# Optimization experiments

Hardware: AMD Instinct MI355X
Metric: run time of the kernel (lower is better)

Reference implementation:

```python
import jax, jax.numpy as jnp
import numpy as np

DOWN = 2
KCONV = 3

def _blur_kernel():
    # _setup_kernel([1,3,3,1]): outer product, normalize; is_ref flips it.
    k = np.array([1.0, 3.0, 3.0, 1.0], dtype=np.float32)
    K = np.outer(k, k)
    K /= K.sum()
    K = K[::-1, ::-1].copy()  # torch.flip(dims=(0,1)) (symmetric here, kept for fidelity)
    return jnp.asarray(K)  # [4,4]

def setup_inputs() -> dict:
    key = jax.random.key(0)
    k1, k2, k3 = jax.random.split(key, 3)
    x = jax.random.normal(k1, (16, 256, 128, 128), dtype=jnp.float32)
    weight = jax.random.normal(k2, (512, 256, KCONV, KCONV), dtype=jnp.float32)  # OIHW
    bias = jax.random.normal(k3, (512,), dtype=jnp.float32)
    return {"x": x, "weight": weight, "bias": bias, "blur_k": _blur_kernel()}

def reference(x, weight, bias, blur_k):
    N, C, H, W = x.shape
    Wb = blur_k.shape[-1]
    # pad sizes: p = Wb - down + (Wconv - 1)
    p = Wb - DOWN + (KCONV - 1)
    pad0, pad1 = (p + 1) // 2, p // 2
    # upfirdn_2d (up=down=1): pad + depthwise FIR correlation with the (pre-flipped) kernel
    kd = jnp.broadcast_to(blur_k[None, None], (C, 1, Wb, Wb))  # depthwise OIHW
    xb = jax.lax.conv_general_dilated(
        x, kd, window_strides=(1, 1),
        padding=[(pad0, pad1), (pad0, pad1)],
        feature_group_count=C,
        dimension_numbers=("NCHW", "OIHW", "NCHW"))  # [N,C,129,129]
    # EqualizedLRConv2d: runtime weight scaling 1/sqrt(fan_in), stride=2, no padding
    fan_in = weight.shape[1] * weight.shape[2] * weight.shape[3]
    scale = 1.0 / np.sqrt(fan_in)
    y = jax.lax.conv_general_dilated(
        xb, weight * jnp.float32(scale), window_strides=(DOWN, DOWN),
        padding="VALID",
        dimension_numbers=("NCHW", "OIHW", "NCHW"))  # [N,512,64,64]
    return y + bias[None, :, None, None]
```

## Files before the change

### kernel.cpp

```cpp
#include <hip/hip_runtime.h>
#include <hip/hip_bf16.h>
#include <stdint.h>
#include <stddef.h>

#define NB   16
#define CIN  256
#define HIN  128
#define WIN  128
#define COUT 512
#define HO   64
#define WO   64
#define HBL  129

typedef __attribute__((ext_vector_type(8))) __bf16 bf16x8;
typedef __attribute__((ext_vector_type(4))) float  f32x4;

__device__ __forceinline__ void gld_lds16(const void* g, void* l) {
  __builtin_amdgcn_global_load_lds(
      (const __attribute__((address_space(1))) void*)g,
      (__attribute__((address_space(3))) void*)l, 16, 0, 0);
}

__device__ __forceinline__ unsigned pack_bf16(float lo, float hi) {
  __hip_bfloat16 l = __float2bfloat16(lo), h = __float2bfloat16(hi);
  unsigned short ul = *(unsigned short*)&l, uh = *(unsigned short*)&h;
  return (unsigned)ul | ((unsigned)uh << 16);
}

__global__ __launch_bounds__(512) void blur_kernel(
    const float* __restrict__ x,
    const float* __restrict__ bk,
    __hip_bfloat16* __restrict__ xb)
{
  __shared__ __hip_bfloat16 lout[CIN * 130];

  const int bid0 = blockIdx.x;
  const int bid  = (bid0 & 7) * 258 + (bid0 >> 3);
  const int n    = bid / HBL;
  const int io   = bid % HBL;
  const int t    = threadIdx.x;
  const int wave = t >> 6;
  const int lane = t & 63;
  const int half = lane >> 5;
  const int g    = lane & 31;

  const float K11 = bk[5];
  float a[4], b[4];
  #pragma unroll
  for (int u = 0; u < 4; ++u) a[u] = bk[u * 4 + 1] / K11;
  #pragma unroll
  for (int v = 0; v < 4; ++v) b[v] = bk[4 + v];

  int rr[4];
  #pragma unroll
  for (int u = 0; u < 4; ++u) {
    int r = io - 2 + u;
    if (r < 0 || r >= HIN) { a[u] = 0.f; r = 0; }
    rr[u] = r;
  }

  #pragma unroll 2
  for (int cb = wave * 2; cb < CIN; cb += 16) {
    const int c = cb + half;
    const float4* xr = (const float4*)(x + ((size_t)(n * CIN + c) * HIN) * WIN);
    float4 vm = {0.f, 0.f, 0.f, 0.f};
    #pragma unroll
    for (int u = 0; u < 4; ++u) {
      const float4 rv = xr[rr[u] * 32 + g];
      vm.x += a[u] * rv.x; vm.y += a[u] * rv.y;
      vm.z += a[u] * rv.z; vm.w += a[u] * rv.w;
    }
    float vmm2 = __shfl_up(vm.z, 1);
    float vmm1 = __shfl_up(vm.w, 1);
    float vmp4 = __shfl_down(vm.x, 1);
    if (g == 0)  { vmm2 = 0.f; vmm1 = 0.f; }
    if (g == 31) { vmp4 = 0.f; }
    const float o0 = b[0]*vmm2 + b[1]*vmm1 + b[2]*vm.x + b[3]*vm.y;
    const float o1 = b[0]*vmm1 + b[1]*vm.x + b[2]*vm.y + b[3]*vm.z;
    const float o2 = b[0]*vm.x + b[1]*vm.y + b[2]*vm.z + b[3]*vm.w;
    const float o3 = b[0]*vm.y + b[1]*vm.z + b[2]*vm.w + b[3]*vmp4;
    unsigned* dst = (unsigned*)&lout[c * 130 + 4 * g];
    dst[0] = pack_bf16(o0, o1);
    dst[1] = pack_bf16(o2, o3);
    if (g == 31)
      lout[c * 130 + 128] = __float2bfloat16(b[0]*vm.z + b[1]*vm.w);
  }

  __syncthreads();

  const size_t obase = ((size_t)(n * HBL + io)) * HBL * CIN;
  for (int e = t; e < 65 * 64; e += 512) {
    const int jp = e >> 6;
    const int l  = e & 63;
    const unsigned r0 = *(const unsigned*)&lout[(4*l + 0) * 130 + 2*jp];
    const unsigned r1 = *(const unsigned*)&lout[(4*l + 1) * 130 + 2*jp];
    const unsigned r2 = *(const unsigned*)&lout[(4*l + 2) * 130 + 2*jp];
    const unsigned r3 = *(const unsigned*)&lout[(4*l + 3) * 130 + 2*jp];
    uint2 s0, s1;
    s0.x = (r0 & 0xffffu) | (r1 << 16);
    s0.y = (r2 & 0xffffu) | (r3 << 16);
    s1.x = (r0 >> 16) | (r1 & 0xffff0000u);
    s1.y = (r2 >> 16) | (r3 & 0xffff0000u);
    *(uint2*)&xb[obase + (size_t)(2*jp) * CIN + 4*l] = s0;
    if (jp < 64)
      *(uint2*)&xb[obase + (size_t)(2*jp + 1) * CIN + 4*l] = s1;
  }
}

__global__ __launch_bounds__(256) void wprep_kernel(
    const float* __restrict__ w,
    __hip_bfloat16* __restrict__ wt)
{
  const int idx = blockIdx.x * 256 + threadIdx.x;
  if (idx >= 9 * COUT * CIN) return;
  const int c   = idx & (CIN - 1);
  const int o   = (idx >> 8) & (COUT - 1);
  const int tap = idx >> 17;
  wt[idx] = __float2bfloat16(w[(o * CIN + c) * 9 + tap]);
}

__global__ void gemm_kernel(
    const __hip_bfloat16* __restrict__ xb,
    const __hip_bfloat16* __restrict__ wt,
    const float* __restrict__ bias,
    float* __restrict__ y)
{
  __shared__ __hip_bfloat16 sW[128 * 64];
  __shared__ __hip_bfloat16 sX[128 * 64];

  const int t    = threadIdx.x;
  const int wave = t >> 6;
  const int lane = t & 63;
  const int bid0 = blockIdx.x;
  const int bid  = (bid0 & 7) * 256 + (bid0 >> 3);
  const int nb   = bid & 3;
  const int mb   = bid >> 2;
  const int o0   = nb * 128;
  const int p0   = mb * 128;
  const int imgn = p0 >> 12;
  const int h0   = (p0 >> 6) & 63;

  const int lane_r = lane >> 3;
  const int lane_g = lane & 7;

  f32x4 acc[4][4];
  #pragma unroll
  for (int ai = 0; ai < 4; ++ai)
    #pragma unroll
    for (int bi = 0; bi < 4; ++bi)
      acc[ai][bi] = (f32x4){0.f, 0.f, 0.f, 0.f};

  long xconst[4], wconst[4];
  #pragma unroll
  for (int s = 0; s < 4; ++s) {
    const int r  = (wave * 4 + s) * 8 + lane_r;
    const int g  = lane_g ^ (r & 7);
    const int hh = h0 + (r >> 6);
    const int ww = r & 63;
    xconst[s] = ((long)(imgn * HBL + 2 * hh) * HBL + 2 * ww) * CIN + g * 8;
    wconst[s] = (long)(o0 + r) * CIN + g * 8;
  }

  const int q   = lane >> 4;
  const int m16 = lane & 15;
  const int ro_base = (wave >> 1) * 64;
  const int rp_base = (wave & 1) * 64;

  for (int tap = 0; tap < 9; ++tap) {
    const long xoff_tap = (long)((tap / 3) * HBL + (tap % 3)) * CIN;
    const long woff_tap = (long)tap * (COUT * CIN);
    for (int cb = 0; cb < CIN; cb += 64) {
      #pragma unroll
      for (int s = 0; s < 4; ++s) {
        const int issue = wave * 4 + s;
        gld_lds16(wt + woff_tap + wconst[s] + cb, (char*)sW + issue * 1024);
        gld_lds16(xb + xoff_tap + xconst[s] + cb, (char*)sX + issue * 1024);
      }
      asm volatile("s_waitcnt vmcnt(0)" ::: "memory");
      __syncthreads();

      #pragma unroll
      for (int kk = 0; kk < 2; ++kk) {
        bf16x8 af[4], bfr[4];
        #pragma unroll
        for (int i4 = 0; i4 < 4; ++i4) {
          const int ro = ro_base + i4 * 16 + m16;
          const int ga = (kk * 4 + q) ^ (ro & 7);
          af[i4] = *(const bf16x8*)((const char*)sW + ro * 128 + ga * 16);
          const int rp = rp_base + i4 * 16 + m16;
          const int gb = (kk * 4 + q) ^ (rp & 7);
          bfr[i4] = *(const bf16x8*)((const char*)sX + rp * 128 + gb * 16);
        }
        #pragma unroll
        for (int ai = 0; ai < 4; ++ai)
          #pragma unroll
          for (int bi = 0; bi < 4; ++bi)
            acc[ai][bi] = __builtin_amdgcn_mfma_f32_16x16x32_bf16(
                af[ai], bfr[bi], acc[ai][bi], 0, 0, 0);
      }
      __syncthreads();
    }
  }

  const float scale = 1.0f / 48.0f;
  #pragma unroll
  for (int ai = 0; ai < 4; ++ai) {
    const int o = o0 + (wave >> 1) * 64 + ai * 16 + q * 4;
    #pragma unroll
    for (int bi = 0; bi < 4; ++bi) {
      const int p  = p0 + (wave & 1) * 64 + bi * 16 + m16;
      const int n  = p >> 12;
      const int hh = (p >> 6) & 63;
      const int ww = p & 63;
      const size_t obase = ((size_t)(n * COUT + o) * HO + hh) * WO + ww;
      #pragma unroll
      for (int rg = 0; rg < 4; ++rg) {
        const float v = acc[ai][bi][rg] * scale + bias[o + rg];
        y[obase + (size_t)rg * (HO * WO)] = v;
      }
    }
  }
}

extern "C" void kernel_launch(void* const* d_in, const int* in_sizes, int n_in,
                              void* d_out, int out_size, void* d_ws, size_t ws_size,
                              hipStream_t stream) {
  const float* x  = (const float*)d_in[0];
  const float* w  = (const float*)d_in[1];
  const float* bs = (const float*)d_in[2];
  const float* bk = (const float*)d_in[3];
  float* y = (float*)d_out;

  __hip_bfloat16* xb = (__hip_bfloat16*)d_ws;
  __hip_bfloat16* wt = (__hip_bfloat16*)((char*)d_ws +
                       (size_t)NB * HBL * HBL * CIN * sizeof(__hip_bfloat16));

  hipLaunchKernelGGL(blur_kernel, dim3(NB * HBL), dim3(512), 0, stream, x, bk, xb);
  hipLaunchKernelGGL(wprep_kernel, dim3((9 * COUT * CIN + 255) / 256), dim3(256), 0, stream, w, wt);
  hipLaunchKernelGGL(gemm_kernel, dim3((65536 / 128) * (COUT / 128)), dim3(256), 0, stream,
                     xb, wt, bs, y);
}
```

Baseline: 603.4 us.

## Enlarge GEMM tile to 256x256 with 4-stage async LDS pipeline

Rewrites the implicit-GEMM conv kernel to use 256x256 output tiles with 512 threads and a K step of 32, so each wave computes 128x64. Loads go through a 4-slot ring of LDS buffers: each iteration issues the fetch three steps ahead, waits on a partial vmcnt, and uses raw s_barrier instead of a full drain every K step. It also raises MFMA wave priority and changes the swizzle. The aim is more data reuse per tile and global-load latency hidden behind MFMA work. In exchange it needs 128KB of LDS and 128 accumulator registers per thread, and leaves only 512 blocks, which may limit occupancy and balance across CUs.

```diff
diff --git a/kernel.cpp b/kernel.cpp
--- a/kernel.cpp
+++ b/kernel.cpp
@@ -119,103 +119,144 @@
   wt[idx] = __float2bfloat16(w[(o * CIN + c) * 9 + tap]);
 }
 
-__global__ void gemm_kernel(
+__global__ __launch_bounds__(512, 2) void gemm_kernel(
     const __hip_bfloat16* __restrict__ xb,
     const __hip_bfloat16* __restrict__ wt,
     const float* __restrict__ bias,
     float* __restrict__ y)
 {
-  __shared__ __hip_bfloat16 sW[128 * 64];
-  __shared__ __hip_bfloat16 sX[128 * 64];
+  __shared__ __align__(16) char lds[4 * 32768];
 
   const int t    = threadIdx.x;
   const int wave = t >> 6;
   const int lane = t & 63;
   const int bid0 = blockIdx.x;
-  const int bid  = (bid0 & 7) * 256 + (bid0 >> 3);
-  const int nb   = bid & 3;
-  const int mb   = bid >> 2;
-  const int o0   = nb * 128;
-  const int p0   = mb * 128;
+  const int bid  = (bid0 & 7) * 64 + (bid0 >> 3);
+  const int nb   = bid & 1;
+  const int mb   = bid >> 1;
+  const int o0   = nb * 256;
+  const int p0   = mb * 256;
   const int imgn = p0 >> 12;
   const int h0   = (p0 >> 6) & 63;
 
-  const int lane_r = lane >> 3;
-  const int lane_g = lane & 7;
-
-  f32x4 acc[4][4];
-  #pragma unroll
-  for (int ai = 0; ai < 4; ++ai)
-    #pragma unroll
-    for (int bi = 0; bi < 4; ++bi)
-      acc[ai][bi] = (f32x4){0.f, 0.f, 0.f, 0.f};
-
-  long xconst[4], wconst[4];
-  #pragma unroll
-  for (int s = 0; s < 4; ++s) {
-    const int r  = (wave * 4 + s) * 8 + lane_r;
-    const int g  = lane_g ^ (r & 7);
+  const int wo  = wave >> 2;
+  const int wp  = wave & 3;
+  const int q   = lane >> 4;
+  const int m16 = lane & 15;
+
+  long xg[2], wg[2];
+  int  ldsoff[2];
+  #pragma unroll
+  for (int s = 0; s < 2; ++s) {
+    const int ia = wave * 2 + s;
+    const int Lr = ia * 8 + (lane >> 3);
+    const int g3 = (lane & 7) ^ (Lr & 7);
+    const int r  = 2 * Lr + (g3 >> 2);
+    const int cq = (g3 & 3) * 8;
     const int hh = h0 + (r >> 6);
     const int ww = r & 63;
-    xconst[s] = ((long)(imgn * HBL + 2 * hh) * HBL + 2 * ww) * CIN + g * 8;
-    wconst[s] = (long)(o0 + r) * CIN + g * 8;
-  }
-
-  const int q   = lane >> 4;
-  const int m16 = lane & 15;
-  const int ro_base = (wave >> 1) * 64;
-  const int rp_base = (wave & 1) * 64;
-
-  for (int tap = 0; tap < 9; ++tap) {
-    const long xoff_tap = (long)((tap / 3) * HBL + (tap % 3)) * CIN;
-    const long woff_tap = (long)tap * (COUT * CIN);
-    for (int cb = 0; cb < CIN; cb += 64) {
+    xg[s] = ((long)(imgn * HBL + 2 * hh) * HBL + 2 * ww) * CIN + cq;
+    wg[s] = (long)(o0 + r) * CIN + cq;
+    ldsoff[s] = ia * 1024;
+  }
+
+  int aoff[8];
+  #pragma unroll
+  for (int of = 0; of < 8; ++of) {
+    const int r  = wo * 128 + of * 16 + m16;
+    const int g3 = (((r & 1) << 2) | q) ^ ((r >> 1) & 7);
+    aoff[of] = (r >> 1) * 128 + g3 * 16;
+  }
+  int boff[4];
+  #pragma unroll
+  for (int pf = 0; pf < 4; ++pf) {
+    const int r  = wp * 64 + pf * 16 + m16;
+    const int g3 = (((r & 1) << 2) | q) ^ ((r >> 1) & 7);
+    boff[pf] = (r >> 1) * 128 + g3 * 16;
+  }
+
+  f32x4 acc[8][4];
+  #pragma unroll
+  for (int of = 0; of < 8; ++of)
+    #pragma unroll
+    for (int pf = 0; pf < 4; ++pf)
+      acc[of][pf] = (f32x4){0.f, 0.f, 0.f, 0.f};
+
+  auto stage = [&](int kt) {
+    const int  slot = kt & 3;
+    const int  tap  = kt >> 3;
+    const int  cb   = (kt & 7) * 32;
+    const long xoff = (long)((tap / 3) * HBL + (tap % 3)) * CIN + cb;
+    const long woff = (long)tap * (COUT * CIN) + cb;
+    char* sb = &lds[slot * 32768];
+    #pragma unroll
+    for (int s = 0; s < 2; ++s) {
+      gld_lds16(wt + woff + wg[s], sb + ldsoff[s]);
+      gld_lds16(xb + xoff + xg[s], sb + 16384 + ldsoff[s]);
+    }
+  };
+
+  auto compute = [&](int kt) {
+    const char* sb = &lds[(kt & 3) * 32768];
+    bf16x8 aw[8], bx[4];
+    #pragma unroll
+    for (int of = 0; of < 8; ++of)
+      aw[of] = *(const bf16x8*)(sb + aoff[of]);
+    #pragma unroll
+    for (int pf = 0; pf < 4; ++pf)
+      bx[pf] = *(const bf16x8*)(sb + 16384 + boff[pf]);
+    __builtin_amdgcn_s_setprio(1);
+    #pragma unroll
+    for (int of = 0; of < 8; ++of)
       #pragma unroll
-      for (int s = 0; s < 4; ++s) {
-        const int issue = wave * 4 + s;
-        gld_lds16(wt + woff_tap + wconst[s] + cb, (char*)sW + issue * 1024);
-        gld_lds16(xb + xoff_tap + xconst[s] + cb, (char*)sX + issue * 1024);
-      }
-      asm volatile("s_waitcnt vmcnt(0)" ::: "memory");
-      __syncthreads();
-
-      #pragma unroll
-      for (int kk = 0; kk < 2; ++kk) {
-        bf16x8 af[4], bfr[4];
-        #pragma unroll
-        for (int i4 = 0; i4 < 4; ++i4) {
-          const int ro = ro_base + i4 * 16 + m16;
-          const int ga = (kk * 4 + q) ^ (ro & 7);
-          af[i4] = *(const bf16x8*)((const char*)sW + ro * 128 + ga * 16);
-          const int rp = rp_base + i4 * 16 + m16;
-          const int gb = (kk * 4 + q) ^ (rp & 7);
-          bfr[i4] = *(const bf16x8*)((const char*)sX + rp * 128 + gb * 16);
-        }
-        #pragma unroll
-        for (int ai = 0; ai < 4; ++ai)
-          #pragma unroll
-          for (int bi = 0; bi < 4; ++bi)
-            acc[ai][bi] = __builtin_amdgcn_mfma_f32_16x16x32_bf16(
-                af[ai], bfr[bi], acc[ai][bi], 0, 0, 0);
-      }
-      __syncthreads();
-    }
-  }
+      for (int pf = 0; pf < 4; ++pf)
+        acc[of][pf] = __builtin_amdgcn_mfma_f32_16x16x32_bf16(
+            aw[of], bx[pf], acc[of][pf], 0, 0, 0);
+    __builtin_amdgcn_s_setprio(0);
+  };
+
+  stage(0); stage(1); stage(2);
+
+  for (int kt = 0; kt < 69; ++kt) {
+    stage(kt + 3);
+    asm volatile("s_waitcnt vmcnt(12)" ::: "memory");
+    __builtin_amdgcn_s_barrier();
+    __builtin_amdgcn_sched_barrier(0);
+    compute(kt);
+    __builtin_amdgcn_sched_barrier(0);
+    __builtin_amdgcn_s_barrier();
+  }
+  asm volatile("s_waitcnt vmcnt(8)" ::: "memory");
+  __builtin_amdgcn_s_barrier();
+  __builtin_amdgcn_sched_barrier(0);
+  compute(69);
+  __builtin_amdgcn_sched_barrier(0);
+  __builtin_amdgcn_s_barrier();
+  asm volatile("s_waitcnt vmcnt(4)" ::: "memory");
+  __builtin_amdgcn_s_barrier();
+  __builtin_amdgcn_sched_barrier(0);
+  compute(70);
+  __builtin_amdgcn_sched_barrier(0);
+  __builtin_amdgcn_s_barrier();
+  asm volatile("s_waitcnt vmcnt(0)" ::: "memory");
+  __builtin_amdgcn_s_barrier();
+  __builtin_amdgcn_sched_barrier(0);
+  compute(71);
 
   const float scale = 1.0f / 48.0f;
   #pragma unroll
-  for (int ai = 0; ai < 4; ++ai) {
-    const int o = o0 + (wave >> 1) * 64 + ai * 16 + q * 4;
-    #pragma unroll
-    for (int bi = 0; bi < 4; ++bi) {
-      const int p  = p0 + (wave & 1) * 64 + bi * 16 + m16;
+  for (int of = 0; of < 8; ++of) {
+    const int o = o0 + wo * 128 + of * 16 + q * 4;
+    #pragma unroll
+    for (int pf = 0; pf < 4; ++pf) {
+      const int p  = p0 + wp * 64 + pf * 16 + m16;
       const int n  = p >> 12;
       const int hh = (p >> 6) & 63;
       const int ww = p & 63;
       const size_t obase = ((size_t)(n * COUT + o) * HO + hh) * WO + ww;
       #pragma unroll
       for (int rg = 0; rg < 4; ++rg) {
-        const float v = acc[ai][bi][rg] * scale + bias[o + rg];
+        const float v = acc[of][pf][rg] * scale + bias[o + rg];
         y[obase + (size_t)rg * (HO * WO)] = v;
       }
     }
@@ -237,6 +278,6 @@
 
   hipLaunchKernelGGL(blur_kernel, dim3(NB * HBL), dim3(512), 0, stream, x, bk, xb);
   hipLaunchKernelGGL(wprep_kernel, dim3((9 * COUT * CIN + 255) / 256), dim3(256), 0, stream, w, wt);
-  hipLaunchKernelGGL(gemm_kernel, dim3((65536 / 128) * (COUT / 128)), dim3(256), 0, stream,
+  hipLaunchKernelGGL(gemm_kernel, dim3(256 * 2), dim3(512), 0, stream,
                      xb, wt, bs, y);
 }
```

Result: faster. 572.9 us (-5.0%).
